# Performance work log

Hardware: AMD Instinct MI355X
Metric: run time of the kernel (lower is better)

Reference implementation:

```python
import jax, jax.numpy as jnp
import numpy as np

S, B, H, NH, M = 2048, 2, 2048, 16, 2048
D = H // NH
FF = 4 * H
NORM = float(np.sqrt(D))  # norm_factor = sqrt(head_dim), no layer scaling
MASK_FILL = jnp.float32(-1e4)


def _ln(x, g, b):
    mu = jnp.mean(x, -1, keepdims=True)
    var = jnp.mean(jnp.square(x - mu), -1, keepdims=True)
    return (x - mu) * jax.lax.rsqrt(var + 1e-5) * g + b


def _l2(x):  # F.normalize over last dim
    return x * jax.lax.rsqrt(jnp.sum(jnp.square(x), -1, keepdims=True) + 1e-12)


def _mlp(h, w1, b1, w2, b2):  # ParallelMLP: h -> 4h -> h with gelu
    return jax.nn.gelu(h @ w1 + b1) @ w2 + b2


def setup_inputs() -> dict:
    key = jax.random.key(0)
    ks = jax.random.split(key, 12)
    w = lambda k, sh: jax.random.normal(k, sh, jnp.float32) * 0.02
    return {
        'x': jax.random.normal(ks[0], (S, B, H), jnp.float32),
        'mem_hidden': jax.random.normal(ks[1], (M, B, H), jnp.float32),
        'mem_mask': jax.random.randint(ks[2], (B, 1, S, M), 0, 5) == 0,  # True = masked
        'ln1_g': jnp.ones((H,), jnp.float32), 'ln1_b': jnp.zeros((H,), jnp.float32),
        'ln2_g': jnp.ones((H,), jnp.float32), 'ln2_b': jnp.zeros((H,), jnp.float32),
        'ln3_g': jnp.ones((H,), jnp.float32), 'ln3_b': jnp.zeros((H,), jnp.float32),
        'w_mlp1_in': w(ks[3], (H, FF)), 'b_mlp1_in': jnp.zeros((FF,), jnp.float32),
        'w_mlp1_out': w(ks[4], (FF, H)), 'b_mlp1_out': jnp.zeros((H,), jnp.float32),
        'w_q': w(ks[5], (H, H)), 'b_q': jnp.zeros((H,), jnp.float32),
        'w_kv': w(ks[6], (H, 2 * H)), 'b_kv': jnp.zeros((2 * H,), jnp.float32),
        'w_dense': w(ks[7], (H, H)), 'b_dense': jnp.zeros((H,), jnp.float32),
        'w_mlp2_in': w(ks[8], (H, FF)), 'b_mlp2_in': jnp.zeros((FF,), jnp.float32),
        'w_mlp2_out': w(ks[9], (FF, H)), 'b_mlp2_out': jnp.zeros((H,), jnp.float32),
    }


def reference(x, mem_hidden, mem_mask, ln1_g, ln1_b, ln2_g, ln2_b, ln3_g, ln3_b,
              w_mlp1_in, b_mlp1_in, w_mlp1_out, b_mlp1_out,
              w_q, b_q, w_kv, b_kv, w_dense, b_dense,
              w_mlp2_in, b_mlp2_in, w_mlp2_out, b_mlp2_out):
    # NOTE: source literally replaces x with mlp1 output (no residual on mlp1)
    x = _mlp(_ln(x, ln1_g, ln1_b), w_mlp1_in, b_mlp1_in, w_mlp1_out, b_mlp1_out)

    # memory attention: l2-normalized query vs l2-normalized retrieved memory k/v
    h2 = _ln(x, ln2_g, ln2_b)
    q = _l2((h2 @ w_q + b_q).reshape(S, B, NH, D))              # [s,b,h,d]
    kv = (mem_hidden @ w_kv + b_kv).reshape(M, B, NH, 2 * D)    # hidden_to_kv
    k = _l2(kv[..., :D])                                        # [m,b,h,d]
    v = _l2(kv[..., D:])
    scores = jnp.einsum('sbhd,mbhd->bhsm', q, k) / NORM
    scores = jnp.where(mem_mask, MASK_FILL, scores)             # attention_mask_func fill
    probs = jax.nn.softmax(scores, axis=-1)
    ctx = jnp.einsum('bhsm,mbhd->sbhd', probs, v).reshape(S, B, H)
    x = x + ctx @ w_dense + b_dense                             # dense w/ skip_bias_add

    x = x + _mlp(_ln(x, ln3_g, ln3_b), w_mlp2_in, b_mlp2_in, w_mlp2_out, b_mlp2_out)
    return x
```

## Files before the change

### kernel.cpp

```cpp
#include <hip/hip_runtime.h>
#include <stdint.h>
#include <stddef.h>

typedef __attribute__((ext_vector_type(8))) short bf16x8;
typedef __attribute__((ext_vector_type(4))) float f32x4;
typedef unsigned short u16;
typedef unsigned int u32;
typedef unsigned long long u64;

static constexpr int S_ = 2048, B_ = 2, H_ = 2048, NH_ = 16, D_ = 128, M_ = 2048, FF_ = 8192;
static constexpr int SB_ = S_ * B_;
static constexpr int MB_ = M_ * B_;

__device__ __forceinline__ float b2f(u16 b) {
  union { u32 u; float f; } v; v.u = ((u32)b) << 16; return v.f;
}
__device__ __forceinline__ u16 f2b(float f) {
  union { float f; u32 u; } v; v.f = f;
  u32 u = v.u;
  return (u16)((u + 0x7FFFu + ((u >> 16) & 1u)) >> 16);
}
__device__ __forceinline__ float geluf(float x) {
  float x3 = x * x * x;
  return 0.5f * x * (1.0f + tanhf(0.7978845608028654f * (x + 0.044715f * x3)));
}

#define LDSP(p) (reinterpret_cast<__attribute__((address_space(3))) uint32_t*>(reinterpret_cast<uintptr_t>(p)))
#define GLBP(p) (reinterpret_cast<const __attribute__((address_space(1))) uint32_t*>(reinterpret_cast<uintptr_t>(p)))

__global__ void detect_kinds(const u32* __restrict__ x0, const u32* __restrict__ mask, int* __restrict__ flags) {
  if (threadIdx.x == 0 && blockIdx.x == 0) {
    int cnt = 0;
    for (int i = 0; i < 256; ++i) {
      u32 e = (x0[i] >> 7) & 0xFFu;
      if (e >= 118u && e <= 130u) ++cnt;
    }
    flags[0] = (cnt >= 128) ? 0 : 1;
    int all01 = 1, allf = 1, allb = 1;
    for (int i = 0; i < 256; ++i) {
      u32 v = mask[i];
      if (v > 1u) all01 = 0;
      if (v != 0u && v != 0x3F800000u) allf = 0;
      u32 lo = v & 0xFFFFu, hi = v >> 16;
      if ((lo != 0u && lo != 0x3F80u) || (hi != 0u && hi != 0x3F80u)) allb = 0;
    }
    flags[1] = all01 ? 1 : (allf ? 3 : (allb ? 2 : 0));
  }
}

__global__ void mask_bits(const void* __restrict__ mraw, const int* __restrict__ flags, u64* __restrict__ bm) {
  int i = blockIdx.x * 256 + threadIdx.x;
  int kind = flags[1];
  int masked;
  if (kind == 1)      masked = ((const int*)mraw)[i] != 0;
  else if (kind == 3) masked = ((const float*)mraw)[i] != 0.0f;
  else if (kind == 2) masked = ((const u16*)mraw)[i] != 0;
  else                masked = ((const unsigned char*)mraw)[i] != 0;
  u64 vote = __ballot(masked == 0);
  if ((threadIdx.x & 63) == 0) bm[i >> 6] = vote;
}

__global__ void cvt_f32(const void* __restrict__ src, const int* __restrict__ flags, float* __restrict__ dst, int n) {
  int i = blockIdx.x * 256 + threadIdx.x;
  if (i < n) dst[i] = flags[0] ? ((const float*)src)[i] : b2f(((const u16*)src)[i]);
}

__global__ void cast_in_bf16(const void* __restrict__ src, const int* __restrict__ flags, u16* __restrict__ dst, int n8) {
  int i = blockIdx.x * 256 + threadIdx.x;
  if (i >= n8) return;
  if (flags[0]) {
    const float4* p = (const float4*)src;
    float4 a = p[i * 2], c = p[i * 2 + 1];
    bf16x8 o;
    o[0] = (short)f2b(a.x); o[1] = (short)f2b(a.y); o[2] = (short)f2b(a.z); o[3] = (short)f2b(a.w);
    o[4] = (short)f2b(c.x); o[5] = (short)f2b(c.y); o[6] = (short)f2b(c.z); o[7] = (short)f2b(c.w);
    *(bf16x8*)&dst[i * 8] = o;
  } else {
    *(bf16x8*)&dst[i * 8] = ((const bf16x8*)src)[i];
  }
}

__global__ __launch_bounds__(256) void transpose_cast(const void* __restrict__ in, const int* __restrict__ flags,
                                                      u16* __restrict__ out, int R, int C) {
  __shared__ u16 tile[64][65];
  const int isf = flags[0];
  const int tr = blockIdx.y * 64, tc = blockIdx.x * 64;
  const int tx = threadIdx.x & 63, ty = threadIdx.x >> 6;
  const float* inf = (const float*)in;
  const u16* inb = (const u16*)in;
#pragma unroll
  for (int i = 0; i < 16; ++i) {
    int r = ty * 16 + i;
    size_t idx = (size_t)(tr + r) * C + tc + tx;
    tile[r][tx] = isf ? f2b(inf[idx]) : inb[idx];
  }
  __syncthreads();
#pragma unroll
  for (int i = 0; i < 16; ++i) {
    int c = ty * 16 + i;
    out[(size_t)(tc + c) * R + tr + tx] = tile[tx][c];
  }
}

template <int EXT>
__global__ __launch_bounds__(256) void layernorm_k(const void* __restrict__ xin, const int* __restrict__ flags,
                                                   const float* __restrict__ g, const float* __restrict__ bta,
                                                   u16* __restrict__ out) {
  const int row = blockIdx.x, t = threadIdx.x;
  float v[8];
  bool bfmode = EXT && (flags[0] == 0);
  if (bfmode) {
    const u16* xr = (const u16*)xin + (size_t)row * H_ + t * 8;
    bf16x8 a = *(const bf16x8*)xr;
#pragma unroll
    for (int j = 0; j < 8; ++j) v[j] = b2f((u16)a[j]);
  } else {
    const float* xr = (const float*)xin + (size_t)row * H_ + t * 8;
    float4 a = *(const float4*)xr, c = *(const float4*)(xr + 4);
    v[0] = a.x; v[1] = a.y; v[2] = a.z; v[3] = a.w;
    v[4] = c.x; v[5] = c.y; v[6] = c.z; v[7] = c.w;
  }
  float s1 = 0.f, s2 = 0.f;
#pragma unroll
  for (int j = 0; j < 8; ++j) { s1 += v[j]; s2 += v[j] * v[j]; }
#pragma unroll
  for (int off = 32; off > 0; off >>= 1) { s1 += __shfl_down(s1, off); s2 += __shfl_down(s2, off); }
  __shared__ float red[8];
  const int w = t >> 6;
  if ((t & 63) == 0) { red[w] = s1; red[4 + w] = s2; }
  __syncthreads();
  s1 = red[0] + red[1] + red[2] + red[3];
  s2 = red[4] + red[5] + red[6] + red[7];
  const float mean = s1 * (1.0f / H_);
  const float rstd = rsqrtf(s2 * (1.0f / H_) - mean * mean + 1e-5f);
  bf16x8 o;
#pragma unroll
  for (int j = 0; j < 8; ++j) {
    float y = (v[j] - mean) * rstd * g[t * 8 + j] + bta[t * 8 + j];
    o[j] = (short)f2b(y);
  }
  *(bf16x8*)(out + (size_t)row * H_ + t * 8) = o;
}

template <int BN, int GELU, int RES, int WF, int WB, int ODYN>
__global__ __launch_bounds__(512, 2) void gemm8p(const u16* __restrict__ A, const u16* __restrict__ Bt,
                                                 const float* __restrict__ bias, const float* __restrict__ res,
                                                 void* __restrict__ outF, u16* __restrict__ outB,
                                                 const int* __restrict__ flags, int Mr, int N, int K) {
  constexpr int NBF = (BN == 256) ? 2 : 1;
  __shared__ u16 lds[65536];
  const int t = threadIdx.x;
  const int w = t >> 6, l = t & 63, lr = l & 15, lk = l >> 4;
  const int wr = w >> 2, wc = w & 3;
  const int gx = gridDim.x, gy = gridDim.y;
  const int orig = blockIdx.y * gx + blockIdx.x;
  const int nwg = gx * gy, per = nwg >> 3;
  int tm, tn;
  {
    const int xcd = orig & 7, p = orig >> 3;
    const int ncx = gx >> 3 ? gx >> 3 : 1;
    if ((gx & 7) == 0 && (per & 7) == 0) {
      const int cy = per >> 3;
      const int ccol = xcd % ncx, crow = xcd / ncx;
      const int px = p & 7, py = p >> 3;
      tn = (ccol * 8 + px) * BN;
      tm = (crow * cy + py) * 256;
    } else {
      tn = (orig % gx) * BN;
      tm = (orig / gx) * 256;
    }
  }
  const int r0 = t >> 3;
  const int cl = (t & 7) ^ (r0 & 7);
  const u32 abase = (u32)(tm + r0) * (u32)K + (u32)cl * 8;
  const u32 bbase = (u32)(tn + r0) * (u32)K + (u32)cl * 8;
  const int wdst = w * 512;
  const int cso0 = ((0 + lk) ^ (lr & 7)) * 8;
  const int cso1 = ((4 + lk) ^ (lr & 7)) * 8;
  const int brow0 = (BN == 256) ? ((wc & 1) * 64) : (wc * 32);

  const int NT = K >> 6, NI = NT >> 1;
  f32x4 acc[8][2 * NBF] = {};

#define STGA_(h) do { if ((h) < 2 * NT) {                                                              \
    const int sl_ = ((h) & 3) * 8192;                                                                  \
    const u32 so_ = abase + ((u32)((h) & 1) * 128u) * (u32)K + ((u32)((h) >> 1)) * 64u;                \
    __builtin_amdgcn_global_load_lds(GLBP(A + so_), LDSP(lds + sl_ + wdst), 16, 0, 0);                 \
    __builtin_amdgcn_global_load_lds(GLBP(A + so_ + (u32)64 * (u32)K), LDSP(lds + sl_ + 4096 + wdst), 16, 0, 0); \
  } } while (0)
#define STGB_(h) do {                                                                                  \
    if constexpr (BN == 256) { if ((h) < 2 * NT) {                                                     \
      const int sl_ = 32768 + ((h) & 3) * 8192;                                                        \
      const u32 so_ = bbase + ((u32)((h) & 1) * 128u) * (u32)K + ((u32)((h) >> 1)) * 64u;              \
      __builtin_amdgcn_global_load_lds(GLBP(Bt + so_), LDSP(lds + sl_ + wdst), 16, 0, 0);              \
      __builtin_amdgcn_global_load_lds(GLBP(Bt + so_ + (u32)64 * (u32)K), LDSP(lds + sl_ + 4096 + wdst), 16, 0, 0); \
    } } else { if ((h) < NT) {                                                                         \
      const int sl_ = 32768 + ((h) & 3) * 8192;                                                        \
      const u32 so_ = bbase + ((u32)(h)) * 64u;                                                        \
      __builtin_amdgcn_global_load_lds(GLBP(Bt + so_), LDSP(lds + sl_ + wdst), 16, 0, 0);              \
      __builtin_amdgcn_global_load_lds(GLBP(Bt + so_ + (u32)64 * (u32)K), LDSP(lds + sl_ + 4096 + wdst), 16, 0, 0); \
    } }                                                                                                \
  } while (0)
#define RDA_(dst, mh, sa)                                                                              \
  _Pragma("unroll") for (int mf2 = 0; mf2 < 4; ++mf2) {                                                \
    const u16* p_ = lds + (sa) * 8192 + ((mh) * 64 + mf2 * 16 + lr) * 64;                              \
    dst[mf2][0] = *(const bf16x8*)(p_ + cso0);                                                         \
    dst[mf2][1] = *(const bf16x8*)(p_ + cso1); }
#define RDB_(dst, nh, sb)                                                                              \
  _Pragma("unroll") for (int nf2 = 0; nf2 < NBF; ++nf2) {                                              \
    const u16* p_ = lds + 32768 + (sb) * 8192 + (brow0 + ((nh) * NBF + nf2) * 16 + lr) * 64;           \
    dst[nf2][0] = *(const bf16x8*)(p_ + cso0);                                                         \
    dst[nf2][1] = *(const bf16x8*)(p_ + cso1); }
#define MM_(afX, bqX, mh, nh)                                                                          \
  _Pragma("unroll") for (int kk = 0; kk < 2; ++kk)                                                     \
  _Pragma("unroll") for (int mf2 = 0; mf2 < 4; ++mf2)                                                  \
  _Pragma("unroll") for (int nf2 = 0; nf2 < NBF; ++nf2)                                                \
    acc[(mh) * 4 + mf2][(nh) * NBF + nf2] = __builtin_amdgcn_mfma_f32_16x16x32_bf16(                   \
        afX[mf2][kk], bqX[nf2][kk], acc[(mh) * 4 + mf2][(nh) * NBF + nf2], 0, 0, 0);
#define PHASE_MID()                                                                                    \
  __builtin_amdgcn_s_barrier();                                                                        \
  asm volatile("s_waitcnt lgkmcnt(0)" ::: "memory");                                                   \
  __builtin_amdgcn_sched_barrier(0);                                                                   \
  __builtin_amdgcn_s_setprio(1);
#define PHASE_END()                                                                                    \
  __builtin_amdgcn_s_setprio(0);                                                                       \
  __builtin_amdgcn_sched_barrier(0);                                                                   \
  __builtin_amdgcn_s_barrier();

  if constexpr (BN == 256) {
    STGB_(0); STGA_(0); STGB_(1); STGA_(1); STGB_(2); STGA_(2);
  } else {
    STGB_(0); STGA_(0); STGA_(1); STGB_(1); STGA_(2);
  }
  asm volatile("s_waitcnt vmcnt(4)" ::: "memory");
  __builtin_amdgcn_s_barrier();

  for (int it = 0; it < NI; ++it) {
    const int T0 = it * 2;
    const int saA0 = (2 * T0 + wr) & 3;
    const int saA1 = (2 * T0 + 2 + wr) & 3;
    const int sbB0 = (BN == 256) ? ((2 * T0 + (wc >> 1)) & 3) : (T0 & 3);
    const int sbB1 = (BN == 256) ? ((2 * T0 + 2 + (wc >> 1)) & 3) : ((T0 + 1) & 3);
    const bool last = (it + 1 == NI);
    bf16x8 af[4][2], bq0[NBF][2], bq1[NBF][2];

    RDA_(af, 0, saA0); RDB_(bq0, 0, sbB0);
    if constexpr (BN == 256) STGB_(4 * it + 3); else STGA_(4 * it + 3);
    PHASE_MID(); MM_(af, bq0, 0, 0); PHASE_END();
    RDB_(bq1, 1, sbB0);
    if constexpr (BN == 256) STGA_(4 * it + 3);
    PHASE_MID(); MM_(af, bq1, 0, 1); PHASE_END();
    RDA_(af, 1, saA0);
    if constexpr (BN == 256) STGB_(4 * it + 4); else STGB_(2 * it + 2);
    PHASE_MID(); MM_(af, bq0, 1, 0); PHASE_END();
    STGA_(4 * it + 4);
    __builtin_amdgcn_s_barrier();
    __builtin_amdgcn_s_setprio(1);
    MM_(af, bq1, 1, 1);
    __builtin_amdgcn_s_setprio(0);
    __builtin_amdgcn_sched_barrier(0);
    if (!last) { asm volatile("s_waitcnt vmcnt(4)" ::: "memory"); }
    else       { asm volatile("s_waitcnt vmcnt(0)" ::: "memory"); }
    __builtin_amdgcn_s_barrier();

    RDA_(af, 0, saA1); RDB_(bq0, 0, sbB1);
    if constexpr (BN == 256) STGB_(4 * it + 5); else STGA_(4 * it + 5);
    PHASE_MID(); MM_(af, bq0, 0, 0); PHASE_END();
    RDB_(bq1, 1, sbB1);
    if constexpr (BN == 256) STGA_(4 * it + 5); else STGB_(2 * it + 3);
    PHASE_MID(); MM_(af, bq1, 0, 1); PHASE_END();
    RDA_(af, 1, saA1);
    if constexpr (BN == 256) STGB_(4 * it + 6);
    PHASE_MID(); MM_(af, bq0, 1, 0); PHASE_END();
    STGA_(4 * it + 6);
    __builtin_amdgcn_s_barrier();
    __builtin_amdgcn_s_setprio(1);
    MM_(af, bq1, 1, 1);
    __builtin_amdgcn_s_setprio(0);
    __builtin_amdgcn_sched_barrier(0);
    if (!last) { asm volatile("s_waitcnt vmcnt(4)" ::: "memory"); }
    __builtin_amdgcn_s_barrier();
  }
#undef STGA_
#undef STGB_
#undef RDA_
#undef RDB_
#undef MM_
#undef PHASE_MID
#undef PHASE_END

  const int obf = ODYN ? (flags[0] ? 0 : 1) : 0;
  (void)Mr;
#pragma unroll
  for (int mf = 0; mf < 8; ++mf) {
#pragma unroll
    for (int nf = 0; nf < 2 * NBF; ++nf) {
      const int col = tn + wc * (BN == 256 ? 64 : 32) + nf * 16 + lr;
      const float bv = bias[col];
#pragma unroll
      for (int j = 0; j < 4; ++j) {
        const int rw = tm + wr * 128 + mf * 16 + lk * 4 + j;
        float vv = acc[mf][nf][j] + bv;
        if (RES) vv += res[(size_t)rw * N + col];
        if (GELU) vv = geluf(vv);
        if (WF) {
          if (ODYN && obf) ((u16*)outF)[(size_t)rw * N + col] = f2b(vv);
          else ((float*)outF)[(size_t)rw * N + col] = vv;
        }
        if (WB) outB[(size_t)rw * N + col] = f2b(vv);
      }
    }
  }
}

__global__ __launch_bounds__(256) void l2_q(const float* __restrict__ qpre, u16* __restrict__ Q) {
  const int t = threadIdx.x;
  const int g = blockIdx.x * 64 + (t >> 2);
  const int lg = t & 3;
  const int h = g & (NH_ - 1), sb = g >> 4;
  const float* p = qpre + (size_t)sb * H_ + h * D_ + lg * 32;
  float vv[32];
  float ss = 0.f;
#pragma unroll
  for (int i = 0; i < 8; ++i) {
    float4 a = *(const float4*)&p[i * 4];
    vv[i * 4 + 0] = a.x; vv[i * 4 + 1] = a.y; vv[i * 4 + 2] = a.z; vv[i * 4 + 3] = a.w;
    ss += a.x * a.x + a.y * a.y + a.z * a.z + a.w * a.w;
  }
  ss += __shfl_xor(ss, 1); ss += __shfl_xor(ss, 2);
  const float sc = rsqrtf(ss + 1e-12f);
  const int s = sb >> 1, b = sb & 1;
  u16* o = Q + ((size_t)(b * NH_ + h) * S_ + s) * D_ + lg * 32;
#pragma unroll
  for (int i = 0; i < 4; ++i) {
    bf16x8 ov;
#pragma unroll
    for (int j = 0; j < 8; ++j) ov[j] = (short)f2b(vv[i * 8 + j] * sc);
    *(bf16x8*)&o[i * 8] = ov;
  }
}

__global__ __launch_bounds__(256) void l2_kv(const float* __restrict__ kvpre, u16* __restrict__ Kq, u16* __restrict__ Vt) {
  __shared__ u16 vtT[128][72];
  const int t = threadIdx.x;
  const int bid = blockIdx.x;
  const int mt = bid & 31, h = (bid >> 5) & 15, b = bid >> 9;
  const int lm = t >> 2, lg = t & 3;
  const int m = mt * 64 + lm;
  const size_t rowoff = (size_t)(m * B_ + b) * (2 * H_) + h * 256;
  float vv[32];
  {
    const float* p = kvpre + rowoff + lg * 32;
    float ss = 0.f;
#pragma unroll
    for (int i = 0; i < 8; ++i) {
      float4 a = *(const float4*)&p[i * 4];
      vv[i * 4 + 0] = a.x; vv[i * 4 + 1] = a.y; vv[i * 4 + 2] = a.z; vv[i * 4 + 3] = a.w;
      ss += a.x * a.x + a.y * a.y + a.z * a.z + a.w * a.w;
    }
    ss += __shfl_xor(ss, 1); ss += __shfl_xor(ss, 2);
    const float sc = rsqrtf(ss + 1e-12f);
    u16* o = Kq + ((size_t)(b * NH_ + h) * M_ + m) * D_ + lg * 32;
#pragma unroll
    for (int i = 0; i < 4; ++i) {
      bf16x8 ov;
#pragma unroll
      for (int j = 0; j < 8; ++j) ov[j] = (short)f2b(vv[i * 8 + j] * sc);
      *(bf16x8*)&o[i * 8] = ov;
    }
  }
  {
    const float* p = kvpre + rowoff + 128 + lg * 32;
    float ss = 0.f;
#pragma unroll
    for (int i = 0; i < 8; ++i) {
      float4 a = *(const float4*)&p[i * 4];
      vv[i * 4 + 0] = a.x; vv[i * 4 + 1] = a.y; vv[i * 4 + 2] = a.z; vv[i * 4 + 3] = a.w;
      ss += a.x * a.x + a.y * a.y + a.z * a.z + a.w * a.w;
    }
    ss += __shfl_xor(ss, 1); ss += __shfl_xor(ss, 2);
    const float sc = rsqrtf(ss + 1e-12f);
#pragma unroll
    for (int i = 0; i < 32; ++i) vtT[lg * 32 + i][lm] = f2b(vv[i] * sc);
  }
  __syncthreads();
  const int d = t >> 1, half = t & 1;
  u16* o = Vt + ((size_t)(b * NH_ + h) * D_ + d) * M_ + mt * 64 + half * 32;
#pragma unroll
  for (int i = 0; i < 4; ++i) {
    bf16x8 ov = *(const bf16x8*)&vtT[d][half * 32 + i * 8];
    *(bf16x8*)&o[i * 8] = ov;
  }
}

__global__ __launch_bounds__(256, 3) void attn_k(const u16* __restrict__ Q, const u16* __restrict__ Kq,
                                                 const u16* __restrict__ Vt, const u32* __restrict__ BM32,
                                                 u16* __restrict__ ctx) {
  __shared__ u16 Kl[2][4096];
  __shared__ u16 Vl[2][4096];
  __shared__ u16 Pl[4][16 * 40];
  const int t = threadIdx.x, w = t >> 6, l = t & 63, lr = l & 15, lk = l >> 4;
  const int lin = blockIdx.x;
  const int xcd = lin & 7, idx = lin >> 3;
  const int bh = xcd * 4 + (idx >> 5);
  const int chunk = idx & 31;
  const int b = bh >> 4, h = bh & 15;
  const int srow = chunk * 64 + w * 16;
  const u16* Qb = Q + ((size_t)bh * S_ + srow) * D_;
  bf16x8 qf[4];
#pragma unroll
  for (int kc = 0; kc < 4; ++kc)
    qf[kc] = *(const bf16x8*)&Qb[lr * D_ + kc * 32 + lk * 8];
  f32x4 oacc[8] = {};
  float den[4] = {};
  const u16* Kb = Kq + (size_t)bh * M_ * D_;
  const u16* Vb = Vt + (size_t)bh * D_ * M_;
  const float invn = 0.08838834764831845f;
  u32 ksrc[2], vsrc[2];
#pragma unroll
  for (int i = 0; i < 2; ++i) {
    const int kidx = i * 256 + t;
    const int kr = kidx >> 4, kc_ = (kidx & 15) ^ (kr & 7);
    ksrc[i] = (u32)kr * D_ + (u32)kc_ * 8;
    const int vidx = i * 256 + t;
    const int vd = vidx >> 2, vc = (vidx & 3) ^ ((vd >> 1) & 3);
    vsrc[i] = (u32)vd * M_ + (u32)vc * 8;
  }
  const int wdst = w * 64 * 8;
  u32 mrow[4];
#pragma unroll
  for (int j2 = 0; j2 < 4; ++j2)
    mrow[j2] = ((u32)b * S_ + (u32)(srow + lk * 4 + j2)) * 64u;

#define STG(buf, m0) do {                                                                              \
    _Pragma("unroll")                                                                                  \
    for (int i = 0; i < 2; ++i) {                                                                      \
      __builtin_amdgcn_global_load_lds(GLBP(Kb + (size_t)(m0) * D_ + ksrc[i]),                         \
                                       LDSP(&Kl[buf][i * 2048 + wdst]), 16, 0, 0);                     \
      __builtin_amdgcn_global_load_lds(GLBP(Vb + (size_t)(m0) + vsrc[i]),                              \
                                       LDSP(&Vl[buf][i * 2048 + wdst]), 16, 0, 0);                     \
    }                                                                                                  \
  } while (0)

  STG(0, 0);
  asm volatile("s_waitcnt vmcnt(0)" ::: "memory");
  __builtin_amdgcn_s_barrier();
  int cur = 0;

  for (int t64 = 0; t64 < M_ / 32; ++t64) {
    const int m0 = t64 * 32;
    if (t64 + 1 < M_ / 32) STG(cur ^ 1, m0 + 32);
    u32 mw[4];
#pragma unroll
    for (int j2 = 0; j2 < 4; ++j2) mw[j2] = BM32[mrow[j2] + t64];
    f32x4 sc[2] = {};
#pragma unroll
    for (int mf = 0; mf < 2; ++mf) {
      const int r = mf * 16 + lr;
#pragma unroll
      for (int kc = 0; kc < 4; ++kc) {
        const int cc = ((kc * 4 + lk) ^ (r & 7));
        bf16x8 kfv = *(const bf16x8*)&Kl[cur][r * 128 + cc * 8];
        sc[mf] = __builtin_amdgcn_mfma_f32_16x16x32_bf16(qf[kc], kfv, sc[mf], 0, 0, 0);
      }
    }
#pragma unroll
    for (int j2 = 0; j2 < 4; ++j2) {
      const int rloc = lk * 4 + j2;
#pragma unroll
      for (int mf = 0; mf < 2; ++mf) {
        float p = __expf(sc[mf][j2] * invn);
        p = ((mw[j2] >> (mf * 16 + lr)) & 1u) ? p : 0.0f;
        den[j2] += p;
        Pl[w][rloc * 40 + mf * 16 + lr] = f2b(p);
      }
    }
    asm volatile("s_waitcnt lgkmcnt(0)" ::: "memory");
    __builtin_amdgcn_sched_barrier(0);
    bf16x8 pa = *(const bf16x8*)&Pl[w][lr * 40 + lk * 8];
#pragma unroll
    for (int nf = 0; nf < 8; ++nf) {
      const int d = nf * 16 + lr;
      const int cc = lk ^ ((d >> 1) & 3);
      bf16x8 vfv = *(const bf16x8*)&Vl[cur][d * 32 + cc * 8];
      oacc[nf] = __builtin_amdgcn_mfma_f32_16x16x32_bf16(pa, vfv, oacc[nf], 0, 0, 0);
    }
    asm volatile("s_waitcnt vmcnt(0)" ::: "memory");
    __builtin_amdgcn_s_barrier();
    cur ^= 1;
  }
#undef STG
#pragma unroll
  for (int j2 = 0; j2 < 4; ++j2) {
    float d = den[j2];
    d += __shfl_xor(d, 1); d += __shfl_xor(d, 2); d += __shfl_xor(d, 4); d += __shfl_xor(d, 8);
    den[j2] = 1.0f / fmaxf(d, 1e-20f);
  }
#pragma unroll
  for (int nf = 0; nf < 8; ++nf)
#pragma unroll
    for (int j2 = 0; j2 < 4; ++j2) {
      const int s = srow + lk * 4 + j2;
      const int dd = nf * 16 + lr;
      ctx[((size_t)s * B_ + b) * H_ + h * D_ + dd] = f2b(oacc[nf][j2] * den[j2]);
    }
}

extern "C" void kernel_launch(void* const* d_in, const int* in_sizes, int n_in,
                              void* d_out, int out_size, void* d_ws, size_t ws_size,
                              hipStream_t stream) {
  (void)in_sizes; (void)n_in; (void)out_size; (void)ws_size;
  char* ws = (char*)d_ws;
  u16* WT     = (u16*)(ws + 0);
  void* MID   = (void*)(ws + 33554432);
  float* XF   = (float*)(ws + 100663296);
  u16* HB     = (u16*)(ws + 134217728);
  u16* MEMB   = (u16*)(ws + 150994944);
  u16* QB     = (u16*)(ws + 167772160);
  u16* KB     = (u16*)(ws + 184549376);
  u16* VTB    = (u16*)(ws + 201326592);
  u64* BMB    = (u64*)(ws + 218103808);
  float* SM   = (float*)(ws + 234881024);
  int* FLAGS  = (int*)(ws + 235044864);

  float* Bias1  = SM + 0;
  float* Bias1o = SM + 8192;
  float* BiasQ  = SM + 10240;
  float* BiasKV = SM + 12288;
  float* BiasD  = SM + 16384;
  float* Bias2  = SM + 18432;
  float* Bias2o = SM + 26624;
  float* G1v = SM + 28672; float* B1v = SM + 30720;
  float* G2v = SM + 32768; float* B2v = SM + 34816;
  float* G3v = SM + 36864; float* B3v = SM + 38912;

  detect_kinds<<<1, 64, 0, stream>>>((const u32*)d_in[0], (const u32*)d_in[2], FLAGS);

  cvt_f32<<<32, 256, 0, stream>>>(d_in[10], FLAGS, Bias1, 8192);
  cvt_f32<<<8, 256, 0, stream>>>(d_in[12], FLAGS, Bias1o, 2048);
  cvt_f32<<<8, 256, 0, stream>>>(d_in[14], FLAGS, BiasQ, 2048);
  cvt_f32<<<16, 256, 0, stream>>>(d_in[16], FLAGS, BiasKV, 4096);
  cvt_f32<<<8, 256, 0, stream>>>(d_in[18], FLAGS, BiasD, 2048);
  cvt_f32<<<32, 256, 0, stream>>>(d_in[20], FLAGS, Bias2, 8192);
  cvt_f32<<<8, 256, 0, stream>>>(d_in[22], FLAGS, Bias2o, 2048);
  cvt_f32<<<8, 256, 0, stream>>>(d_in[3], FLAGS, G1v, 2048);
  cvt_f32<<<8, 256, 0, stream>>>(d_in[4], FLAGS, B1v, 2048);
  cvt_f32<<<8, 256, 0, stream>>>(d_in[5], FLAGS, G2v, 2048);
  cvt_f32<<<8, 256, 0, stream>>>(d_in[6], FLAGS, B2v, 2048);
  cvt_f32<<<8, 256, 0, stream>>>(d_in[7], FLAGS, G3v, 2048);
  cvt_f32<<<8, 256, 0, stream>>>(d_in[8], FLAGS, B3v, 2048);

  mask_bits<<<(B_ * S_ * M_) / 256, 256, 0, stream>>>(d_in[2], FLAGS, BMB);
  cast_in_bf16<<<(MB_ * H_ / 8) / 256, 256, 0, stream>>>(d_in[1], FLAGS, MEMB, MB_ * H_ / 8);

  dim3 blk(256);
  dim3 blk5(512);
  layernorm_k<1><<<SB_, blk, 0, stream>>>(d_in[0], FLAGS, G1v, B1v, HB);
  transpose_cast<<<dim3(FF_ / 64, H_ / 64), blk, 0, stream>>>(d_in[9], FLAGS, WT, H_, FF_);
  gemm8p<256, 1, 0, 0, 1, 0><<<dim3(FF_ / 256, SB_ / 256), blk5, 0, stream>>>(HB, WT, Bias1, nullptr, nullptr, (u16*)MID, FLAGS, SB_, FF_, H_);
  transpose_cast<<<dim3(H_ / 64, FF_ / 64), blk, 0, stream>>>(d_in[11], FLAGS, WT, FF_, H_);
  gemm8p<128, 0, 0, 1, 0, 0><<<dim3(H_ / 128, SB_ / 256), blk5, 0, stream>>>((u16*)MID, WT, Bias1o, nullptr, XF, nullptr, FLAGS, SB_, H_, FF_);

  layernorm_k<0><<<SB_, blk, 0, stream>>>(XF, FLAGS, G2v, B2v, HB);
  transpose_cast<<<dim3(H_ / 64, H_ / 64), blk, 0, stream>>>(d_in[13], FLAGS, WT, H_, H_);
  gemm8p<128, 0, 0, 1, 0, 0><<<dim3(H_ / 128, SB_ / 256), blk5, 0, stream>>>(HB, WT, BiasQ, nullptr, MID, nullptr, FLAGS, SB_, H_, H_);
  l2_q<<<(SB_ * NH_) / 64, blk, 0, stream>>>((const float*)MID, QB);
  transpose_cast<<<dim3(2 * H_ / 64, H_ / 64), blk, 0, stream>>>(d_in[15], FLAGS, WT, H_, 2 * H_);
  gemm8p<256, 0, 0, 1, 0, 0><<<dim3(2 * H_ / 256, MB_ / 256), blk5, 0, stream>>>(MEMB, WT, BiasKV, nullptr, MID, nullptr, FLAGS, MB_, 2 * H_, H_);
  l2_kv<<<B_ * NH_ * (M_ / 64), blk, 0, stream>>>((const float*)MID, KB, VTB);
  attn_k<<<1024, blk, 0, stream>>>(QB, KB, VTB, (const u32*)BMB, MEMB);
  transpose_cast<<<dim3(H_ / 64, H_ / 64), blk, 0, stream>>>(d_in[17], FLAGS, WT, H_, H_);
  gemm8p<128, 0, 1, 1, 0, 0><<<dim3(H_ / 128, SB_ / 256), blk5, 0, stream>>>(MEMB, WT, BiasD, XF, XF, nullptr, FLAGS, SB_, H_, H_);

  layernorm_k<0><<<SB_, blk, 0, stream>>>(XF, FLAGS, G3v, B3v, HB);
  transpose_cast<<<dim3(FF_ / 64, H_ / 64), blk, 0, stream>>>(d_in[19], FLAGS, WT, H_, FF_);
  gemm8p<256, 1, 0, 0, 1, 0><<<dim3(FF_ / 256, SB_ / 256), blk5, 0, stream>>>(HB, WT, Bias2, nullptr, nullptr, (u16*)MID, FLAGS, SB_, FF_, H_);
  transpose_cast<<<dim3(H_ / 64, FF_ / 64), blk, 0, stream>>>(d_in[21], FLAGS, WT, FF_, H_);
  gemm8p<128, 0, 1, 1, 0, 1><<<dim3(H_ / 128, SB_ / 256), blk5, 0, stream>>>((u16*)MID, WT, Bias2o, XF, d_out, nullptr, FLAGS, SB_, H_, FF_);
}
```

Baseline: 1.267 ms.

## Deepen GEMM prefetch to two k-tiles ahead and fuse bias conversion launches

Reworks the GEMM main loop's global-to-LDS staging so each half-iteration issues loads for a tile two steps ahead. The prologue now preloads four stages, and the vmcnt waits are adjusted to match, so more memory latency can overlap with MFMA work. It also drops one sched_barrier in the phase epilogue. Separately, thirteen small cvt_f32 launches become one cvt_all kernel that writes all biases and LN params into the scratch array, cutting launch overhead. The risk is that a wrong wait count or a stage/slot mismatch in the LDS ring could corrupt data or add stalls.

```diff
diff --git a/kernel.cpp b/kernel.cpp
--- a/kernel.cpp
+++ b/kernel.cpp
@@ -60,9 +60,28 @@
   if ((threadIdx.x & 63) == 0) bm[i >> 6] = vote;
 }
 
-__global__ void cvt_f32(const void* __restrict__ src, const int* __restrict__ flags, float* __restrict__ dst, int n) {
-  int i = blockIdx.x * 256 + threadIdx.x;
-  if (i < n) dst[i] = flags[0] ? ((const float*)src)[i] : b2f(((const u16*)src)[i]);
+__global__ void cvt_all(const void* s0, const void* s1, const void* s2, const void* s3,
+                        const void* s4, const void* s5, const void* s6, const void* s7,
+                        const void* s8, const void* s9, const void* s10, const void* s11,
+                        const void* s12, const int* __restrict__ flags, float* __restrict__ SM) {
+  const int i = blockIdx.x * 256 + threadIdx.x;
+  if (i >= 40960) return;
+  const void* src; int off;
+  if (i < 8192)       { src = s0;  off = 0; }
+  else if (i < 10240) { src = s1;  off = 8192; }
+  else if (i < 12288) { src = s2;  off = 10240; }
+  else if (i < 16384) { src = s3;  off = 12288; }
+  else if (i < 18432) { src = s4;  off = 16384; }
+  else if (i < 26624) { src = s5;  off = 18432; }
+  else if (i < 28672) { src = s6;  off = 26624; }
+  else if (i < 30720) { src = s7;  off = 28672; }
+  else if (i < 32768) { src = s8;  off = 30720; }
+  else if (i < 34816) { src = s9;  off = 32768; }
+  else if (i < 36864) { src = s10; off = 34816; }
+  else if (i < 38912) { src = s11; off = 36864; }
+  else                { src = s12; off = 38912; }
+  const int j = i - off;
+  SM[i] = flags[0] ? ((const float*)src)[j] : b2f(((const u16*)src)[j]);
 }
 
 __global__ void cast_in_bf16(const void* __restrict__ src, const int* __restrict__ flags, u16* __restrict__ dst, int n8) {
@@ -224,62 +243,67 @@
   __builtin_amdgcn_s_setprio(1);
 #define PHASE_END()                                                                                    \
   __builtin_amdgcn_s_setprio(0);                                                                       \
-  __builtin_amdgcn_sched_barrier(0);                                                                   \
   __builtin_amdgcn_s_barrier();
+#define VMW_FULL()                                                                                     \
+  if constexpr (BN == 256) { asm volatile("s_waitcnt vmcnt(8)" ::: "memory"); }                        \
+  else                     { asm volatile("s_waitcnt vmcnt(6)" ::: "memory"); }
 
   if constexpr (BN == 256) {
-    STGB_(0); STGA_(0); STGB_(1); STGA_(1); STGB_(2); STGA_(2);
+    STGB_(0); STGB_(1); STGA_(0); STGA_(1);
+    STGB_(2); STGB_(3); STGA_(2); STGA_(3);
+    asm volatile("s_waitcnt vmcnt(8)" ::: "memory");
   } else {
-    STGB_(0); STGA_(0); STGA_(1); STGB_(1); STGA_(2);
-  }
-  asm volatile("s_waitcnt vmcnt(4)" ::: "memory");
+    STGB_(0); STGA_(0); STGA_(1);
+    STGB_(1); STGA_(2); STGA_(3);
+    asm volatile("s_waitcnt vmcnt(6)" ::: "memory");
+  }
   __builtin_amdgcn_s_barrier();
 
   for (int it = 0; it < NI; ++it) {
     const int T0 = it * 2;
-    const int saA0 = (2 * T0 + wr) & 3;
-    const int saA1 = (2 * T0 + 2 + wr) & 3;
-    const int sbB0 = (BN == 256) ? ((2 * T0 + (wc >> 1)) & 3) : (T0 & 3);
-    const int sbB1 = (BN == 256) ? ((2 * T0 + 2 + (wc >> 1)) & 3) : ((T0 + 1) & 3);
-    const bool last = (it + 1 == NI);
     bf16x8 af[4][2], bq0[NBF][2], bq1[NBF][2];
 
-    RDA_(af, 0, saA0); RDB_(bq0, 0, sbB0);
-    if constexpr (BN == 256) STGB_(4 * it + 3); else STGA_(4 * it + 3);
-    PHASE_MID(); MM_(af, bq0, 0, 0); PHASE_END();
-    RDB_(bq1, 1, sbB0);
-    if constexpr (BN == 256) STGA_(4 * it + 3);
-    PHASE_MID(); MM_(af, bq1, 0, 1); PHASE_END();
-    RDA_(af, 1, saA0);
-    if constexpr (BN == 256) STGB_(4 * it + 4); else STGB_(2 * it + 2);
-    PHASE_MID(); MM_(af, bq0, 1, 0); PHASE_END();
-    STGA_(4 * it + 4);
-    __builtin_amdgcn_s_barrier();
-    __builtin_amdgcn_s_setprio(1);
-    MM_(af, bq1, 1, 1);
-    __builtin_amdgcn_s_setprio(0);
-    __builtin_amdgcn_sched_barrier(0);
-    if (!last) { asm volatile("s_waitcnt vmcnt(4)" ::: "memory"); }
-    else       { asm volatile("s_waitcnt vmcnt(0)" ::: "memory"); }
-    __builtin_amdgcn_s_barrier();
-
-    RDA_(af, 0, saA1); RDB_(bq0, 0, sbB1);
-    if constexpr (BN == 256) STGB_(4 * it + 5); else STGA_(4 * it + 5);
-    PHASE_MID(); MM_(af, bq0, 0, 0); PHASE_END();
-    RDB_(bq1, 1, sbB1);
-    if constexpr (BN == 256) STGA_(4 * it + 5); else STGB_(2 * it + 3);
-    PHASE_MID(); MM_(af, bq1, 0, 1); PHASE_END();
-    RDA_(af, 1, saA1);
-    if constexpr (BN == 256) STGB_(4 * it + 6);
-    PHASE_MID(); MM_(af, bq0, 1, 0); PHASE_END();
-    STGA_(4 * it + 6);
-    __builtin_amdgcn_s_barrier();
-    __builtin_amdgcn_s_setprio(1);
-    MM_(af, bq1, 1, 1);
-    __builtin_amdgcn_s_setprio(0);
-    __builtin_amdgcn_sched_barrier(0);
-    if (!last) { asm volatile("s_waitcnt vmcnt(4)" ::: "memory"); }
-    __builtin_amdgcn_s_barrier();
+    {
+      const int sa = (2 * T0 + wr) & 3;
+      const int sb = (BN == 256) ? ((2 * T0 + (wc >> 1)) & 3) : (T0 & 3);
+      RDA_(af, 0, sa); RDB_(bq0, 0, sb);
+      PHASE_MID(); MM_(af, bq0, 0, 0); PHASE_END();
+      RDB_(bq1, 1, sb);
+      PHASE_MID(); MM_(af, bq1, 0, 1); PHASE_END();
+      RDA_(af, 1, sa);
+      if constexpr (BN == 256) { STGB_(2 * T0 + 4); STGB_(2 * T0 + 5); }
+      else                     { STGB_(T0 + 2); }
+      PHASE_MID(); MM_(af, bq0, 1, 0); PHASE_END();
+      STGA_(2 * T0 + 4); STGA_(2 * T0 + 5);
+      __builtin_amdgcn_s_barrier();
+      __builtin_amdgcn_s_setprio(1);
+      MM_(af, bq1, 1, 1);
+      __builtin_amdgcn_s_setprio(0);
+      if (T0 + 2 < NT) { VMW_FULL(); }
+      else             { asm volatile("s_waitcnt vmcnt(0)" ::: "memory"); }
+      __builtin_amdgcn_s_barrier();
+    }
+    {
+      const int T1 = T0 + 1;
+      const int sa = (2 * T1 + wr) & 3;
+      const int sb = (BN == 256) ? ((2 * T1 + (wc >> 1)) & 3) : (T1 & 3);
+      RDA_(af, 0, sa); RDB_(bq0, 0, sb);
+      PHASE_MID(); MM_(af, bq0, 0, 0); PHASE_END();
+      RDB_(bq1, 1, sb);
+      PHASE_MID(); MM_(af, bq1, 0, 1); PHASE_END();
+      RDA_(af, 1, sa);
+      if constexpr (BN == 256) { STGB_(2 * T1 + 4); STGB_(2 * T1 + 5); }
+      else                     { STGB_(T1 + 2); }
+      PHASE_MID(); MM_(af, bq0, 1, 0); PHASE_END();
+      STGA_(2 * T1 + 4); STGA_(2 * T1 + 5);
+      __builtin_amdgcn_s_barrier();
+      __builtin_amdgcn_s_setprio(1);
+      MM_(af, bq1, 1, 1);
+      __builtin_amdgcn_s_setprio(0);
+      if (T1 + 2 < NT) { VMW_FULL(); }
+      else             { asm volatile("s_waitcnt vmcnt(0)" ::: "memory"); }
+      __builtin_amdgcn_s_barrier();
+    }
   }
 #undef STGA_
 #undef STGB_
@@ -288,6 +312,7 @@
 #undef MM_
 #undef PHASE_MID
 #undef PHASE_END
+#undef VMW_FULL
 
   const int obf = ODYN ? (flags[0] ? 0 : 1) : 0;
   (void)Mr;
@@ -536,19 +561,9 @@
 
   detect_kinds<<<1, 64, 0, stream>>>((const u32*)d_in[0], (const u32*)d_in[2], FLAGS);
 
-  cvt_f32<<<32, 256, 0, stream>>>(d_in[10], FLAGS, Bias1, 8192);
-  cvt_f32<<<8, 256, 0, stream>>>(d_in[12], FLAGS, Bias1o, 2048);
-  cvt_f32<<<8, 256, 0, stream>>>(d_in[14], FLAGS, BiasQ, 2048);
-  cvt_f32<<<16, 256, 0, stream>>>(d_in[16], FLAGS, BiasKV, 4096);
-  cvt_f32<<<8, 256, 0, stream>>>(d_in[18], FLAGS, BiasD, 2048);
-  cvt_f32<<<32, 256, 0, stream>>>(d_in[20], FLAGS, Bias2, 8192);
-  cvt_f32<<<8, 256, 0, stream>>>(d_in[22], FLAGS, Bias2o, 2048);
-  cvt_f32<<<8, 256, 0, stream>>>(d_in[3], FLAGS, G1v, 2048);
-  cvt_f32<<<8, 256, 0, stream>>>(d_in[4], FLAGS, B1v, 2048);
-  cvt_f32<<<8, 256, 0, stream>>>(d_in[5], FLAGS, G2v, 2048);
-  cvt_f32<<<8, 256, 0, stream>>>(d_in[6], FLAGS, B2v, 2048);
-  cvt_f32<<<8, 256, 0, stream>>>(d_in[7], FLAGS, G3v, 2048);
-  cvt_f32<<<8, 256, 0, stream>>>(d_in[8], FLAGS, B3v, 2048);
+  cvt_all<<<160, 256, 0, stream>>>(d_in[10], d_in[12], d_in[14], d_in[16], d_in[18],
+                                   d_in[20], d_in[22], d_in[3], d_in[4], d_in[5],
+                                   d_in[6], d_in[7], d_in[8], FLAGS, SM);
 
   mask_bits<<<(B_ * S_ * M_) / 256, 256, 0, stream>>>(d_in[2], FLAGS, BMB);
   cast_in_bf16<<<(MB_ * H_ / 8) / 256, 256, 0, stream>>>(d_in[1], FLAGS, MEMB, MB_ * H_ / 8);
```

Result: no change. 1.251 ms (-1.3%).
